# Kernel optimization log

Hardware: AMD Instinct MI355X
Metric: run time of the kernel (lower is better)

The kernel has to match this reference:

```python
import jax, jax.numpy as jnp
import numpy as np

DIM = 192
STATE = 64
B = 8
H = 64
W = 64
EPS_LN = 1e-5
EPS_BN = 1e-5


def _layernorm(x, g, b):
    m = jnp.mean(x, axis=-1, keepdims=True)
    v = jnp.mean((x - m) ** 2, axis=-1, keepdims=True)
    return (x - m) / jnp.sqrt(v + EPS_LN) * g + b


def _linear(x, w, b=None):
    # torch Linear convention: w is [out, in]
    y = jnp.einsum('...i,oi->...o', x, w)
    return y if b is None else y + b


def _parallel_scan(A, Bd, xp):
    # A, Bd, xp: [B, L, S]; h_t = A_t*h_{t-1} + Bd_t*xp_t via log-space cumsum
    A_safe = jnp.clip(A, 0.001, 0.999)
    log_A = jnp.log(A_safe + 1e-10)
    log_cum_A = jnp.cumsum(log_A, axis=1)
    log_cum_A_max = jnp.max(log_cum_A, axis=1, keepdims=True)
    cum_A = jnp.exp(log_cum_A - log_cum_A_max)
    BX = Bd * xp
    # prepend zeros, drop last: normalizer uses cumprod up to t-1
    log_pad = jnp.pad(log_cum_A - log_cum_A_max, ((0, 0), (1, 0), (0, 0)))[:, :-1]
    BX_norm = BX * jnp.exp(-log_pad)
    return jnp.cumsum(BX_norm, axis=1) * cum_A


def _ssm(x, ln_g, ln_b, xp_w, xp_b, dt_w, dt_b, A_log, B_w, C_w, Dp, out_w, out_b):
    xn = _layernorm(x, ln_g, ln_b)
    delta = jax.nn.softplus(_linear(xn, dt_w, dt_b)) * 0.01 + 0.0001  # [B,L,S]
    B_t = _linear(xn, B_w)
    C_t = _linear(xn, C_w)
    A = -jnp.exp(A_log)  # [S]
    x_proj = _linear(xn, xp_w, xp_b)
    deltaA = jnp.clip(delta * A, -10.0, -0.0001)
    A_disc = jnp.exp(deltaA)
    B_disc = delta * B_t
    h = _parallel_scan(A_disc, B_disc, x_proj)
    y = C_t * h
    y = jnp.where(jnp.all(jnp.isfinite(y)), y, jnp.zeros_like(y))
    y = _linear(y, out_w, out_b)
    return y + jnp.clip(Dp, -2.0, 2.0) * x


def reference(x, ln1_g, ln1_b, ln2_g, ln2_b, dw_w, bn_g, bn_b, bn_rm, bn_rv,
              ssm_ln_g, ssm_ln_b, xp_w, xp_b, dt_w, dt_b, A_log, B_w, C_w,
              D_param, out_w, out_b, mlp_w1, mlp_b1, mlp_w2, mlp_b2,
              alpha_local, alpha_ssm, alpha_mlp):
    identity = x
    # depthwise 3x3 conv + BatchNorm2d (eval mode, running stats)
    xc = jax.lax.conv_general_dilated(
        x, dw_w, (1, 1), 'SAME', feature_group_count=DIM,
        dimension_numbers=('NCHW', 'OIHW', 'NCHW'))
    scale = (bn_g / jnp.sqrt(bn_rv + EPS_BN))[None, :, None, None]
    x_local = (xc - bn_rm[None, :, None, None]) * scale + bn_b[None, :, None, None]
    # SSM branch on flattened spatial sequence
    x_seq = x.transpose(0, 2, 3, 1).reshape(B, H * W, DIM)
    x_seq = _layernorm(x_seq, ln1_g, ln1_b)
    x_seq = _ssm(x_seq, ssm_ln_g, ssm_ln_b, xp_w, xp_b, dt_w, dt_b, A_log,
                 B_w, C_w, D_param, out_w, out_b)
    x_ssm = x_seq.reshape(B, H, W, DIM).transpose(0, 3, 1, 2)
    xr = identity + alpha_local * x_local + alpha_ssm * x_ssm
    # residual MLP (dropout = identity at inference)
    x_mlp = xr.transpose(0, 2, 3, 1).reshape(B, H * W, DIM)
    x_mlp = _layernorm(x_mlp, ln2_g, ln2_b)
    x_mlp = _linear(jax.nn.gelu(_linear(x_mlp, mlp_w1, mlp_b1), approximate=False),
                    mlp_w2, mlp_b2)
    return xr + alpha_mlp * x_mlp.reshape(B, H, W, DIM).transpose(0, 3, 1, 2)


def setup_inputs() -> dict:
    key = jax.random.key(0)
    ks = jax.random.split(key, 12)
    def nrm(k, shape, s):
        return jax.random.normal(k, shape, jnp.float32) * s
    f32 = jnp.float32
    return {
        'x': jax.random.normal(ks[0], (B, DIM, H, W), f32),
        'ln1_g': jnp.ones(DIM, f32), 'ln1_b': jnp.zeros(DIM, f32),
        'ln2_g': jnp.ones(DIM, f32), 'ln2_b': jnp.zeros(DIM, f32),
        'dw_w': nrm(ks[1], (DIM, 1, 3, 3), 0.2),
        'bn_g': jnp.ones(DIM, f32), 'bn_b': jnp.zeros(DIM, f32),
        'bn_rm': jnp.zeros(DIM, f32), 'bn_rv': jnp.ones(DIM, f32),
        'ssm_ln_g': jnp.ones(DIM, f32), 'ssm_ln_b': jnp.zeros(DIM, f32),
        'xp_w': nrm(ks[2], (STATE, DIM), 0.05), 'xp_b': jnp.zeros(STATE, f32),
        'dt_w': nrm(ks[3], (STATE, DIM), 0.05), 'dt_b': jnp.zeros(STATE, f32),
        'A_log': jnp.log(jax.random.uniform(ks[4], (STATE,), f32) * 0.8 + 0.2),
        'B_w': nrm(ks[5], (STATE, DIM), 0.05),
        'C_w': nrm(ks[6], (STATE, DIM), 0.05),
        'D_param': jnp.zeros(DIM, f32),
        'out_w': nrm(ks[7], (DIM, STATE), 0.05), 'out_b': jnp.zeros(DIM, f32),
        'mlp_w1': nrm(ks[8], (4 * DIM, DIM), 0.03), 'mlp_b1': jnp.zeros(4 * DIM, f32),
        'mlp_w2': nrm(ks[9], (DIM, 4 * DIM), 0.03), 'mlp_b2': jnp.zeros(DIM, f32),
        'alpha_local': jnp.full((1,), 0.5, f32),
        'alpha_ssm': jnp.full((1,), 0.5, f32),
        'alpha_mlp': jnp.full((1,), 0.5, f32),
    }
```

## Files before the change

### kernel.cpp

```cpp
#include <hip/hip_runtime.h>
#include <hip/hip_bf16.h>
#include <math.h>


#define DEV static __device__ __forceinline__

constexpr int Bn = 8, Dm = 192, Ln = 4096, Sn = 64, Hd = 768;

typedef __attribute__((ext_vector_type(8))) short bf16x8;
typedef __attribute__((ext_vector_type(4))) float f32x4;

DEV float wave_sum(float v) {
#pragma unroll
  for (int off = 1; off < 64; off <<= 1) v += __shfl_xor(v, off);
  return v;
}

DEV short f2b(float x) {
  __hip_bfloat16 h = __float2bfloat16(x);
  return *(short*)&h;
}

DEV float b2f(short x) {
  __hip_bfloat16 h = *(__hip_bfloat16*)&x;
  return __bfloat162float(h);
}

__global__ __launch_bounds__(256) void k_prep(
    const float* __restrict__ x, const float* __restrict__ g1, const float* __restrict__ b1,
    const float* __restrict__ g2, const float* __restrict__ b2,
    short* __restrict__ xnb, short* __restrict__ xln1b,
    const float* __restrict__ dt_w, const float* __restrict__ B_w,
    const float* __restrict__ C_w, const float* __restrict__ xp_w,
    const float* __restrict__ out_w, const float* __restrict__ w1,
    const float* __restrict__ w2, short* __restrict__ wb) {
  __shared__ __align__(16) float tile[Dm * 65];
  int tid = threadIdx.x;
  if (blockIdx.y == 8) {
    for (int i = blockIdx.x * 256 + tid; i < 89088; i += 64 * 256) {
      const float4* src;
      if (i < 3072)       src = (const float4*)dt_w + i;
      else if (i < 6144)  src = (const float4*)B_w + (i - 3072);
      else if (i < 9216)  src = (const float4*)C_w + (i - 6144);
      else if (i < 12288) src = (const float4*)xp_w + (i - 9216);
      else if (i < 15360) src = (const float4*)out_w + (i - 12288);
      else if (i < 52224) src = (const float4*)w1 + (i - 15360);
      else                src = (const float4*)w2 + (i - 52224);
      float4 v = *src;
      int o = i * 4;
      wb[o] = f2b(v.x); wb[o + 1] = f2b(v.y); wb[o + 2] = f2b(v.z); wb[o + 3] = f2b(v.w);
    }
    return;
  }
  int b = blockIdx.y, l0 = blockIdx.x * 64;
  const float* xb = x + (size_t)b * Dm * Ln;
  for (int i = tid; i < Dm * 16; i += 256) {
    int d = i >> 4, l4 = (i & 15) << 2;
    float4 v = *(const float4*)&xb[d * Ln + l0 + l4];
    tile[d * 65 + l4]     = v.x; tile[d * 65 + l4 + 1] = v.y;
    tile[d * 65 + l4 + 2] = v.z; tile[d * 65 + l4 + 3] = v.w;
  }
  __syncthreads();
  int lane = tid & 63, wv = tid >> 6;
  float ga0 = g1[lane], ga1 = g1[lane + 64], ga2 = g1[lane + 128];
  float bb0 = b1[lane], bb1 = b1[lane + 64], bb2 = b1[lane + 128];
  float gc0 = g2[lane], gc1 = g2[lane + 64], gc2 = g2[lane + 128];
  float bc0 = b2[lane], bc1 = b2[lane + 64], bc2 = b2[lane + 128];
  for (int li = wv; li < 64; li += 4) {
    float v0 = tile[lane * 65 + li], v1 = tile[(lane + 64) * 65 + li], v2 = tile[(lane + 128) * 65 + li];
    float s  = wave_sum(v0 + v1 + v2);
    float sq = wave_sum(v0 * v0 + v1 * v1 + v2 * v2);
    float m = s * (1.f / 192.f);
    float inv = rsqrtf(sq * (1.f / 192.f) - m * m + 1e-5f);
    float y0 = (v0 - m) * inv * ga0 + bb0;
    float y1 = (v1 - m) * inv * ga1 + bb1;
    float y2 = (v2 - m) * inv * ga2 + bb2;
    float s2  = wave_sum(y0 + y1 + y2);
    float sq2 = wave_sum(y0 * y0 + y1 * y1 + y2 * y2);
    float m2 = s2 * (1.f / 192.f);
    float inv2 = rsqrtf(sq2 * (1.f / 192.f) - m2 * m2 + 1e-5f);
    size_t base = ((size_t)b * Ln + l0 + li) * Dm;
    xln1b[base + lane]       = f2b(y0);
    xln1b[base + lane + 64]  = f2b(y1);
    xln1b[base + lane + 128] = f2b(y2);
    xnb[base + lane]       = f2b((y0 - m2) * inv2 * gc0 + bc0);
    xnb[base + lane + 64]  = f2b((y1 - m2) * inv2 * gc1 + bc1);
    xnb[base + lane + 128] = f2b((y2 - m2) * inv2 * gc2 + bc2);
  }
}

__global__ __launch_bounds__(256) void k_proj(
    const short* __restrict__ xnb, const short* __restrict__ wcat,
    const float* __restrict__ dt_b, const float* __restrict__ xp_b,
    const float* __restrict__ A_log, float* __restrict__ aA, unsigned* __restrict__ bxc,
    float* __restrict__ sums) {
  __shared__ __align__(16) short As[64 * 72];
  __shared__ __align__(16) short Bs[256 * 72];
  int m0 = blockIdx.x * 64, tid = threadIdx.x;
  int lane = tid & 63, l16 = lane & 15, quad = lane >> 4, w = tid >> 6;
  f32x4 acc[16] = {};
  for (int kt = 0; kt < 3; kt++) {
    int kb = kt * 64;
    for (int i = tid; i < 512; i += 256) {
      int row = i >> 3, c8 = (i & 7) * 8;
      *(float4*)&As[row * 72 + c8] = *(const float4*)&xnb[(size_t)(m0 + row) * 192 + kb + c8];
    }
    for (int i = tid; i < 2048; i += 256) {
      int row = i >> 3, c8 = (i & 7) * 8;
      *(float4*)&Bs[row * 72 + c8] = *(const float4*)&wcat[(size_t)row * 192 + kb + c8];
    }
    __syncthreads();
#pragma unroll
    for (int ks = 0; ks < 2; ks++) {
      int ko = ks * 32 + quad * 8;
      bf16x8 a0 = *(const bf16x8*)&As[(w * 16 + l16) * 72 + ko];
#pragma unroll
      for (int nh = 0; nh < 2; nh++) {
        bf16x8 bfr[8];
#pragma unroll
        for (int j = 0; j < 8; j++) bfr[j] = *(const bf16x8*)&Bs[((nh * 8 + j) * 16 + l16) * 72 + ko];
#pragma unroll
        for (int j = 0; j < 8; j++)
          acc[nh * 8 + j] = __builtin_amdgcn_mfma_f32_16x16x32_bf16(a0, bfr[j], acc[nh * 8 + j], 0, 0, 0);
      }
    }
    __syncthreads();
  }
  float* aAs = (float*)Bs;
  float* bxs = aAs + 64 * 65;
  float Av[4], dtbv[4], xpbv[4];
#pragma unroll
  for (int ni = 0; ni < 4; ni++) {
    int s = ni * 16 + l16;
    Av[ni] = -expf(A_log[s]); dtbv[ni] = dt_b[s]; xpbv[ni] = xp_b[s];
  }
#pragma unroll
  for (int r = 0; r < 4; r++) {
    int lm = w * 16 + quad * 4 + r;
    int m = m0 + lm;
#pragma unroll
    for (int ni = 0; ni < 4; ni++) {
      int s = ni * 16 + l16;
      float z = acc[ni][r] + dtbv[ni];
      float sp = (z > 20.f) ? z : log1pf(expf(z));
      float delta = sp * 0.01f + 0.0001f;
      float bt  = acc[ni + 4][r];
      float ct  = acc[ni + 8][r];
      float xpv = acc[ni + 12][r] + xpbv[ni];
      float dA = fminf(fmaxf(delta * Av[ni], -10.f), -0.0001f);
      float Ae = fminf(fmaxf(expf(dA), 0.001f), 0.999f) + 1e-10f;
      short bxh = f2b(delta * bt * xpv);
      aA[(size_t)m * 64 + s] = Ae;
      unsigned pk = (unsigned)(unsigned short)bxh
                  | ((unsigned)(unsigned short)f2b(ct) << 16);
      bxc[(size_t)m * 64 + s] = pk;
      aAs[lm * 65 + s] = Ae;
      bxs[lm * 65 + s] = b2f(bxh);
    }
  }
  __syncthreads();
  int s = tid & 63, seg = tid >> 6, chunk = seg >> 1, sub = seg & 1;
  bool first = ((m0 & 4095) == 0) && (chunk == 0) && (sub == 0);
  float P = 1.f, H = 0.f;
  int base = chunk * 32 + sub * 16;
#pragma unroll
  for (int j = 0; j < 16; j++) {
    float a  = aAs[(base + j) * 65 + s];
    float bx = bxs[(base + j) * 65 + s];
    if (first && j == 0) { P = a; H = bx; }
    else { P *= a; H = a * (H + bx); }
  }
  float* partP = (float*)As;
  float* partH = partP + 256;
  partP[seg * 64 + s] = P; partH[seg * 64 + s] = H;
  __syncthreads();
  if (tid < 128) {
    int c = tid >> 6;
    float p0 = partP[(c * 2) * 64 + s], p1 = partP[(c * 2 + 1) * 64 + s];
    float h0 = partH[(c * 2) * 64 + s], h1 = partH[(c * 2 + 1) * 64 + s];
    int ci = (m0 >> 12) * 128 + ((m0 & 4095) >> 5) + c;
    sums[(ci * 2 + 0) * 64 + s] = p0 * p1;
    sums[(ci * 2 + 1) * 64 + s] = p1 * h0 + h1;
  }
}

__global__ __launch_bounds__(256) void k_scan2(const float* __restrict__ sums,
                                               float* __restrict__ carries) {
  __shared__ float Pp[4 * 64], Hp[4 * 64];
  int b = blockIdx.x, tid = threadIdx.x, s = tid & 63, q = tid >> 6;
  float P = 1.f, H = 0.f;
#pragma unroll 4
  for (int j = 0; j < 32; j++) {
    int ci = b * 128 + q * 32 + j;
    float a = sums[(ci * 2 + 0) * 64 + s];
    float h = sums[(ci * 2 + 1) * 64 + s];
    P *= a; H = a * H + h;
  }
  Pp[q * 64 + s] = P; Hp[q * 64 + s] = H;
  __syncthreads();
  float cur = 0.f;
  for (int qq = 0; qq < q; qq++) cur = Pp[qq * 64 + s] * cur + Hp[qq * 64 + s];
#pragma unroll 4
  for (int j = 0; j < 32; j++) {
    int ci = b * 128 + q * 32 + j;
    carries[ci * 64 + s] = cur;
    float a = sums[(ci * 2 + 0) * 64 + s];
    float h = sums[(ci * 2 + 1) * 64 + s];
    cur = a * cur + h;
  }
}

__global__ __launch_bounds__(256) void k_out(
    const float* __restrict__ aA, const unsigned* __restrict__ bxc,
    const float* __restrict__ carries,
    const short* __restrict__ owb, const float* __restrict__ out_b,
    const float* __restrict__ Dp, const short* __restrict__ xln1b, float* __restrict__ sout) {
  __shared__ __align__(16) short As[192 * 72];
  __shared__ __align__(16) short Bs[64 * 72];
  int l0g = blockIdx.x * 64, tid = threadIdx.x;
  int lane = tid & 63, l16 = lane & 15, quad = lane >> 4, wv = tid >> 6;
  for (int i = tid; i < 1536; i += 256) {
    int row = i >> 3, c8 = (i & 7) * 8;
    *(float4*)&As[row * 72 + c8] = *(const float4*)&owb[row * 64 + c8];
  }
  int bb = l0g >> 12, c0 = (l0g & 4095) >> 5;
  if (wv < 2) {
    int c = c0 + wv, s = lane;
    float h = carries[(bb * 128 + c) * 64 + s];
    const float* ap = aA + (size_t)(l0g + wv * 32) * 64;
    const unsigned* bp = bxc + (size_t)(l0g + wv * 32) * 64;
    int t = 0;
    if (c == 0) {
      unsigned u = bp[s];
      h = b2f((short)(u & 0xFFFF));
      Bs[(wv * 32) * 72 + s] = f2b(b2f((short)(u >> 16)) * h);
      t = 1;
    }
#pragma unroll 4
    for (; t < 32; t++) {
      unsigned u = bp[t * 64 + s];
      float a = ap[t * 64 + s];
      h = a * (h + b2f((short)(u & 0xFFFF)));
      Bs[(wv * 32 + t) * 72 + s] = f2b(b2f((short)(u >> 16)) * h);
    }
  }
  __syncthreads();
  f32x4 acc[3][4] = {};
#pragma unroll
  for (int ks = 0; ks < 2; ks++) {
    int ko = ks * 32 + quad * 8;
    bf16x8 a[3], b[4];
#pragma unroll
    for (int mi = 0; mi < 3; mi++) a[mi] = *(const bf16x8*)&As[(wv * 48 + mi * 16 + l16) * 72 + ko];
#pragma unroll
    for (int ni = 0; ni < 4; ni++) b[ni] = *(const bf16x8*)&Bs[(ni * 16 + l16) * 72 + ko];
#pragma unroll
    for (int mi = 0; mi < 3; mi++)
#pragma unroll
      for (int ni = 0; ni < 4; ni++)
        acc[mi][ni] = __builtin_amdgcn_mfma_f32_16x16x32_bf16(a[mi], b[ni], acc[mi][ni], 0, 0, 0);
  }
#pragma unroll
  for (int mi = 0; mi < 3; mi++)
#pragma unroll
    for (int r = 0; r < 4; r++) {
      int d = wv * 48 + mi * 16 + quad * 4 + r;
      float ob = out_b[d];
      float dc = fminf(fmaxf(Dp[d], -2.f), 2.f);
#pragma unroll
      for (int ni = 0; ni < 4; ni++) {
        int l = l0g + ni * 16 + l16;
        float v = acc[mi][ni][r] + ob;
        if (dc != 0.f) v += dc * b2f(xln1b[(size_t)l * 192 + d]);
        sout[((size_t)bb * Dm + d) * Ln + (l & 4095)] = v;
      }
    }
}

__global__ __launch_bounds__(256) void k_conv(
    const float* __restrict__ x, const float* __restrict__ dw,
    const float* __restrict__ bn_g, const float* __restrict__ bn_b,
    const float* __restrict__ bn_rm, const float* __restrict__ bn_rv,
    const float* __restrict__ sout, const float* __restrict__ a_loc,
    const float* __restrict__ a_ssm, float* __restrict__ xr) {
  __shared__ __align__(16) float xs[64 * 64];
  int d = blockIdx.x, b = blockIdx.y, tid = threadIdx.x;
  const float* xp = x + ((size_t)b * Dm + d) * Ln;
  for (int i = tid; i < 1024; i += 256) ((float4*)xs)[i] = ((const float4*)xp)[i];
  __syncthreads();
  float w[9];
#pragma unroll
  for (int k = 0; k < 9; k++) w[k] = dw[d * 9 + k];
  float scale = bn_g[d] * rsqrtf(bn_rv[d] + 1e-5f);
  float rm = bn_rm[d], bb = bn_b[d];
  float al = a_loc[0], as_ = a_ssm[0];
  const float* sp = sout + ((size_t)b * Dm + d) * Ln;
  float* xo = xr + ((size_t)b * Dm + d) * Ln;
  for (int i = tid; i < 4096; i += 256) {
    int h = i >> 6, wc = i & 63;
    float acc = 0.f;
#pragma unroll
    for (int kh = 0; kh < 3; kh++) {
      int hh = h + kh - 1;
      if (hh < 0 || hh >= 64) continue;
#pragma unroll
      for (int kw = 0; kw < 3; kw++) {
        int ww2 = wc + kw - 1;
        if (ww2 < 0 || ww2 >= 64) continue;
        acc += xs[hh * 64 + ww2] * w[kh * 3 + kw];
      }
    }
    float xl = (acc - rm) * scale + bb;
    xo[i] = xs[i] + al * xl + as_ * sp[i];
  }
}

__global__ __launch_bounds__(256) void k_ln2(
    const float* __restrict__ xr, const float* __restrict__ g, const float* __restrict__ bb,
    short* __restrict__ xn2) {
  __shared__ __align__(16) float tile[Dm * 65];
  int b = blockIdx.y, l0 = blockIdx.x * 64, tid = threadIdx.x;
  const float* xb = xr + (size_t)b * Dm * Ln;
  for (int i = tid; i < Dm * 16; i += 256) {
    int d = i >> 4, l4 = (i & 15) << 2;
    float4 v = *(const float4*)&xb[d * Ln + l0 + l4];
    tile[d * 65 + l4]     = v.x; tile[d * 65 + l4 + 1] = v.y;
    tile[d * 65 + l4 + 2] = v.z; tile[d * 65 + l4 + 3] = v.w;
  }
  __syncthreads();
  int lane = tid & 63, wv = tid >> 6;
  float g0 = g[lane], g1v = g[lane + 64], g2v = g[lane + 128];
  float b0 = bb[lane], b1v = bb[lane + 64], b2v = bb[lane + 128];
  for (int li = wv; li < 64; li += 4) {
    float v0 = tile[lane * 65 + li], v1 = tile[(lane + 64) * 65 + li], v2 = tile[(lane + 128) * 65 + li];
    float s  = wave_sum(v0 + v1 + v2);
    float sq = wave_sum(v0 * v0 + v1 * v1 + v2 * v2);
    float m = s * (1.f / 192.f);
    float inv = rsqrtf(sq * (1.f / 192.f) - m * m + 1e-5f);
    size_t base = ((size_t)b * Ln + l0 + li) * Dm;
    xn2[base + lane]       = f2b((v0 - m) * inv * g0 + b0);
    xn2[base + lane + 64]  = f2b((v1 - m) * inv * g1v + b1v);
    xn2[base + lane + 128] = f2b((v2 - m) * inv * g2v + b2v);
  }
}

__global__ __launch_bounds__(256) void k_gemm1(
    const short* __restrict__ xn2, const short* __restrict__ w1b,
    const float* __restrict__ b1h, short* __restrict__ hid) {
  __shared__ __align__(16) short smem[2 * 128 * 88];
  short* As = smem;
  short* Bs = smem + 128 * 88;
  int m0 = blockIdx.x * 128, n0 = blockIdx.y * 128, tid = threadIdx.x;
  int lane = tid & 63, l16 = lane & 15, quad = lane >> 4;
  int wm = (tid >> 6) >> 1, wn = (tid >> 6) & 1;
  f32x4 acc[4][4] = {};
  for (int kt = 0; kt < 3; kt++) {
    int kb = kt * 64;
    for (int i = tid; i < 1024; i += 256) {
      int row = i >> 3, c8 = (i & 7) * 8;
      *(float4*)&As[row * 88 + c8] = *(const float4*)&xn2[(size_t)(m0 + row) * 192 + kb + c8];
      *(float4*)&Bs[row * 88 + c8] = *(const float4*)&w1b[(size_t)(n0 + row) * 192 + kb + c8];
    }
    __syncthreads();
#pragma unroll
    for (int ks = 0; ks < 2; ks++) {
      int ko = ks * 32 + quad * 8;
      bf16x8 a[4], b[4];
#pragma unroll
      for (int mi = 0; mi < 4; mi++) a[mi] = *(const bf16x8*)&As[(wm * 64 + mi * 16 + l16) * 88 + ko];
#pragma unroll
      for (int ni = 0; ni < 4; ni++) b[ni] = *(const bf16x8*)&Bs[(wn * 64 + ni * 16 + l16) * 88 + ko];
#pragma unroll
      for (int mi = 0; mi < 4; mi++)
#pragma unroll
        for (int ni = 0; ni < 4; ni++)
          acc[mi][ni] = __builtin_amdgcn_mfma_f32_16x16x32_bf16(a[mi], b[ni], acc[mi][ni], 0, 0, 0);
    }
    __syncthreads();
  }
  short* Cs = smem;
  float bias4[4];
#pragma unroll
  for (int ni = 0; ni < 4; ni++) bias4[ni] = b1h[n0 + wn * 64 + ni * 16 + l16];
#pragma unroll
  for (int mi = 0; mi < 4; mi++)
#pragma unroll
    for (int ni = 0; ni < 4; ni++) {
      int n = wn * 64 + ni * 16 + l16;
#pragma unroll
      for (int r = 0; r < 4; r++) {
        int m = wm * 64 + mi * 16 + quad * 4 + r;
        float v = acc[mi][ni][r] + bias4[ni];
        float g = 0.5f * v * (1.f + erff(v * 0.70710678118f));
        Cs[m * 136 + n] = f2b(g);
      }
    }
  __syncthreads();
  for (int i = tid; i < 2048; i += 256) {
    int m = i >> 4, ch = i & 15;
    *(float4*)&hid[(size_t)(m0 + m) * 768 + n0 + ch * 8] = *(const float4*)&Cs[m * 136 + ch * 8];
  }
}

__global__ __launch_bounds__(256) void k_gemm2(
    const short* __restrict__ hid, const short* __restrict__ w2b,
    const float* __restrict__ b2o, const float* __restrict__ xr,
    const float* __restrict__ am, float* __restrict__ out) {
  __shared__ __align__(16) short Wt[96 * 88];
  __shared__ __align__(16) short Ht[64 * 88];
  int l0g = blockIdx.x * 64, d0 = blockIdx.y * 96, tid = threadIdx.x;
  int lane = tid & 63, l16 = lane & 15, quad = lane >> 4;
  int wm = (tid >> 6) >> 1, wn = (tid >> 6) & 1;
  f32x4 acc[3][2] = {};
  for (int kt = 0; kt < 12; kt++) {
    int kb = kt * 64;
    for (int i = tid; i < 768; i += 256) {
      int row = i >> 3, c8 = (i & 7) * 8;
      *(float4*)&Wt[row * 88 + c8] = *(const float4*)&w2b[(size_t)(d0 + row) * 768 + kb + c8];
    }
    for (int i = tid; i < 512; i += 256) {
      int row = i >> 3, c8 = (i & 7) * 8;
      *(float4*)&Ht[row * 88 + c8] = *(const float4*)&hid[(size_t)(l0g + row) * 768 + kb + c8];
    }
    __syncthreads();
#pragma unroll
    for (int ks = 0; ks < 2; ks++) {
      int ko = ks * 32 + quad * 8;
      bf16x8 a[3], b[2];
#pragma unroll
      for (int mi = 0; mi < 3; mi++) a[mi] = *(const bf16x8*)&Wt[(wm * 48 + mi * 16 + l16) * 88 + ko];
#pragma unroll
      for (int ni = 0; ni < 2; ni++) b[ni] = *(const bf16x8*)&Ht[(wn * 32 + ni * 16 + l16) * 88 + ko];
#pragma unroll
      for (int mi = 0; mi < 3; mi++)
#pragma unroll
        for (int ni = 0; ni < 2; ni++)
          acc[mi][ni] = __builtin_amdgcn_mfma_f32_16x16x32_bf16(a[mi], b[ni], acc[mi][ni], 0, 0, 0);
    }
    __syncthreads();
  }
  float alpha = am[0];
#pragma unroll
  for (int mi = 0; mi < 3; mi++)
#pragma unroll
    for (int r = 0; r < 4; r++) {
      int d = d0 + wm * 48 + mi * 16 + quad * 4 + r;
      float bias = b2o[d];
#pragma unroll
      for (int ni = 0; ni < 2; ni++) {
        int lg = l0g + wn * 32 + ni * 16 + l16;
        size_t idx = ((size_t)(lg >> 12) * Dm + d) * Ln + (lg & 4095);
        out[idx] = xr[idx] + alpha * (acc[mi][ni][r] + bias);
      }
    }
}

extern "C" void kernel_launch(void* const* d_in, const int* in_sizes, int n_in,
                              void* d_out, int out_size, void* d_ws, size_t ws_size,
                              hipStream_t stream) {
  (void)in_sizes; (void)n_in; (void)out_size; (void)ws_size;
  const float* x     = (const float*)d_in[0];
  const float* ln1_g = (const float*)d_in[1];
  const float* ln1_b = (const float*)d_in[2];
  const float* ln2_g = (const float*)d_in[3];
  const float* ln2_b = (const float*)d_in[4];
  const float* dw_w  = (const float*)d_in[5];
  const float* bn_g  = (const float*)d_in[6];
  const float* bn_b  = (const float*)d_in[7];
  const float* bn_rm = (const float*)d_in[8];
  const float* bn_rv = (const float*)d_in[9];
  const float* ssm_g = (const float*)d_in[10];
  const float* ssm_b = (const float*)d_in[11];
  const float* xp_w  = (const float*)d_in[12];
  const float* xp_b  = (const float*)d_in[13];
  const float* dt_w  = (const float*)d_in[14];
  const float* dt_b  = (const float*)d_in[15];
  const float* A_log = (const float*)d_in[16];
  const float* B_w   = (const float*)d_in[17];
  const float* C_w   = (const float*)d_in[18];
  const float* Dp    = (const float*)d_in[19];
  const float* out_w = (const float*)d_in[20];
  const float* out_b = (const float*)d_in[21];
  const float* w1    = (const float*)d_in[22];
  const float* b1    = (const float*)d_in[23];
  const float* w2    = (const float*)d_in[24];
  const float* b2    = (const float*)d_in[25];
  const float* a_loc = (const float*)d_in[26];
  const float* a_ssm = (const float*)d_in[27];
  const float* a_mlp = (const float*)d_in[28];

  float* ws = (float*)d_ws;
  short*    xnb   = (short*)ws;
  short*    xln1b = (short*)(ws + 3145728);
  float*    aA    = ws + 6291456;
  unsigned* bxc   = (unsigned*)(ws + 8388608);
  float*    sout  = ws + 11534336;
  float*    xr    = ws + 17825792;
  short*    wb    = (short*)(ws + 24117248);
  float*    sums  = ws + 24829952;
  float*    carr  = ws + 24961024;
  short*    xn2   = (short*)(ws + 25026560);
  short*    hid   = (short*)(ws + 28172288);
  short*    wcatb = wb;
  short*    owb   = wb + 49152;
  short*    w1b   = wb + 61440;
  short*    w2b   = wb + 208896;
  float*    out   = (float*)d_out;

  k_prep <<<dim3(64, 9),  256, 0, stream>>>(x, ln1_g, ln1_b, ssm_g, ssm_b, xnb, xln1b,
                                            dt_w, B_w, C_w, xp_w, out_w, w1, w2, wb);
  k_proj <<<dim3(512),    256, 0, stream>>>(xnb, wcatb, dt_b, xp_b, A_log, aA, bxc, sums);
  k_scan2<<<dim3(8),      256, 0, stream>>>(sums, carr);
  k_out  <<<dim3(512),    256, 0, stream>>>(aA, bxc, carr, owb, out_b, Dp, xln1b, sout);
  k_conv <<<dim3(192, 8), 256, 0, stream>>>(x, dw_w, bn_g, bn_b, bn_rm, bn_rv, sout, a_loc, a_ssm, xr);
  k_ln2  <<<dim3(64, 8),  256, 0, stream>>>(xr, ln2_g, ln2_b, xn2);
  k_gemm1<<<dim3(256, 6), 256, 0, stream>>>(xn2, w1b, b1, hid);
  k_gemm2<<<dim3(512, 2), 256, 0, stream>>>(hid, w2b, b2, xr, a_mlp, out);
}
```

Before: 271.7 us.

## Fuse SSM residual add and LayerNorm2 into k_out, run conv first

```diff
diff --git a/kernel.cpp b/kernel.cpp
--- a/kernel.cpp
+++ b/kernel.cpp
@@ -210,13 +210,54 @@
   }
 }
 
+__global__ __launch_bounds__(256) void k_conv(
+    const float* __restrict__ x, const float* __restrict__ dw,
+    const float* __restrict__ bn_g, const float* __restrict__ bn_b,
+    const float* __restrict__ bn_rm, const float* __restrict__ bn_rv,
+    const float* __restrict__ a_loc, float* __restrict__ xr) {
+  __shared__ __align__(16) float xs[64 * 64];
+  int d = blockIdx.x, b = blockIdx.y, tid = threadIdx.x;
+  const float* xp = x + ((size_t)b * Dm + d) * Ln;
+  for (int i = tid; i < 1024; i += 256) ((float4*)xs)[i] = ((const float4*)xp)[i];
+  __syncthreads();
+  float w[9];
+#pragma unroll
+  for (int k = 0; k < 9; k++) w[k] = dw[d * 9 + k];
+  float scale = bn_g[d] * rsqrtf(bn_rv[d] + 1e-5f);
+  float rm = bn_rm[d], bb = bn_b[d];
+  float al = a_loc[0];
+  float* xo = xr + ((size_t)b * Dm + d) * Ln;
+  for (int i = tid; i < 4096; i += 256) {
+    int h = i >> 6, wc = i & 63;
+    float acc = 0.f;
+#pragma unroll
+    for (int kh = 0; kh < 3; kh++) {
+      int hh = h + kh - 1;
+      if (hh < 0 || hh >= 64) continue;
+#pragma unroll
+      for (int kw = 0; kw < 3; kw++) {
+        int ww2 = wc + kw - 1;
+        if (ww2 < 0 || ww2 >= 64) continue;
+        acc += xs[hh * 64 + ww2] * w[kh * 3 + kw];
+      }
+    }
+    float xl = (acc - rm) * scale + bb;
+    xo[i] = xs[i] + al * xl;
+  }
+}
+
 __global__ __launch_bounds__(256) void k_out(
     const float* __restrict__ aA, const unsigned* __restrict__ bxc,
     const float* __restrict__ carries,
     const short* __restrict__ owb, const float* __restrict__ out_b,
-    const float* __restrict__ Dp, const short* __restrict__ xln1b, float* __restrict__ sout) {
-  __shared__ __align__(16) short As[192 * 72];
-  __shared__ __align__(16) short Bs[64 * 72];
+    const float* __restrict__ Dp, const short* __restrict__ xln1b,
+    const float* __restrict__ a_ssm, const float* __restrict__ g2,
+    const float* __restrict__ bb2,
+    float* __restrict__ xr, short* __restrict__ xn2) {
+  __shared__ __align__(16) float smemf[64 * 193];
+  short* As = (short*)smemf;
+  short* Bs = (short*)smemf + 192 * 72;
+  float* tile = smemf;
   int l0g = blockIdx.x * 64, tid = threadIdx.x;
   int lane = tid & 63, l16 = lane & 15, quad = lane >> 4, wv = tid >> 6;
   for (int i = tid; i < 1536; i += 256) {
@@ -260,6 +301,8 @@
       for (int ni = 0; ni < 4; ni++)
         acc[mi][ni] = __builtin_amdgcn_mfma_f32_16x16x32_bf16(a[mi], b[ni], acc[mi][ni], 0, 0, 0);
   }
+  __syncthreads();
+  float as_ = a_ssm[0];
 #pragma unroll
   for (int mi = 0; mi < 3; mi++)
 #pragma unroll
@@ -272,72 +315,22 @@
         int l = l0g + ni * 16 + l16;
         float v = acc[mi][ni][r] + ob;
         if (dc != 0.f) v += dc * b2f(xln1b[(size_t)l * 192 + d]);
-        sout[((size_t)bb * Dm + d) * Ln + (l & 4095)] = v;
+        size_t idx = ((size_t)bb * Dm + d) * Ln + (l & 4095);
+        float nx = xr[idx] + as_ * v;
+        xr[idx] = nx;
+        tile[(l & 63) * 193 + d] = nx;
       }
     }
-}
-
-__global__ __launch_bounds__(256) void k_conv(
-    const float* __restrict__ x, const float* __restrict__ dw,
-    const float* __restrict__ bn_g, const float* __restrict__ bn_b,
-    const float* __restrict__ bn_rm, const float* __restrict__ bn_rv,
-    const float* __restrict__ sout, const float* __restrict__ a_loc,
-    const float* __restrict__ a_ssm, float* __restrict__ xr) {
-  __shared__ __align__(16) float xs[64 * 64];
-  int d = blockIdx.x, b = blockIdx.y, tid = threadIdx.x;
-  const float* xp = x + ((size_t)b * Dm + d) * Ln;
-  for (int i = tid; i < 1024; i += 256) ((float4*)xs)[i] = ((const float4*)xp)[i];
-  __syncthreads();
-  float w[9];
-#pragma unroll
-  for (int k = 0; k < 9; k++) w[k] = dw[d * 9 + k];
-  float scale = bn_g[d] * rsqrtf(bn_rv[d] + 1e-5f);
-  float rm = bn_rm[d], bb = bn_b[d];
-  float al = a_loc[0], as_ = a_ssm[0];
-  const float* sp = sout + ((size_t)b * Dm + d) * Ln;
-  float* xo = xr + ((size_t)b * Dm + d) * Ln;
-  for (int i = tid; i < 4096; i += 256) {
-    int h = i >> 6, wc = i & 63;
-    float acc = 0.f;
-#pragma unroll
-    for (int kh = 0; kh < 3; kh++) {
-      int hh = h + kh - 1;
-      if (hh < 0 || hh >= 64) continue;
-#pragma unroll
-      for (int kw = 0; kw < 3; kw++) {
-        int ww2 = wc + kw - 1;
-        if (ww2 < 0 || ww2 >= 64) continue;
-        acc += xs[hh * 64 + ww2] * w[kh * 3 + kw];
-      }
-    }
-    float xl = (acc - rm) * scale + bb;
-    xo[i] = xs[i] + al * xl + as_ * sp[i];
-  }
-}
-
-__global__ __launch_bounds__(256) void k_ln2(
-    const float* __restrict__ xr, const float* __restrict__ g, const float* __restrict__ bb,
-    short* __restrict__ xn2) {
-  __shared__ __align__(16) float tile[Dm * 65];
-  int b = blockIdx.y, l0 = blockIdx.x * 64, tid = threadIdx.x;
-  const float* xb = xr + (size_t)b * Dm * Ln;
-  for (int i = tid; i < Dm * 16; i += 256) {
-    int d = i >> 4, l4 = (i & 15) << 2;
-    float4 v = *(const float4*)&xb[d * Ln + l0 + l4];
-    tile[d * 65 + l4]     = v.x; tile[d * 65 + l4 + 1] = v.y;
-    tile[d * 65 + l4 + 2] = v.z; tile[d * 65 + l4 + 3] = v.w;
-  }
-  __syncthreads();
-  int lane = tid & 63, wv = tid >> 6;
-  float g0 = g[lane], g1v = g[lane + 64], g2v = g[lane + 128];
-  float b0 = bb[lane], b1v = bb[lane + 64], b2v = bb[lane + 128];
+  __syncthreads();
+  float g0 = g2[lane], g1v = g2[lane + 64], g2v = g2[lane + 128];
+  float b0 = bb2[lane], b1v = bb2[lane + 64], b2v = bb2[lane + 128];
   for (int li = wv; li < 64; li += 4) {
-    float v0 = tile[lane * 65 + li], v1 = tile[(lane + 64) * 65 + li], v2 = tile[(lane + 128) * 65 + li];
+    float v0 = tile[li * 193 + lane], v1 = tile[li * 193 + lane + 64], v2 = tile[li * 193 + lane + 128];
     float s  = wave_sum(v0 + v1 + v2);
     float sq = wave_sum(v0 * v0 + v1 * v1 + v2 * v2);
     float m = s * (1.f / 192.f);
     float inv = rsqrtf(sq * (1.f / 192.f) - m * m + 1e-5f);
-    size_t base = ((size_t)b * Ln + l0 + li) * Dm;
+    size_t base = (size_t)(l0g + li) * Dm;
     xn2[base + lane]       = f2b((v0 - m) * inv * g0 + b0);
     xn2[base + lane + 64]  = f2b((v1 - m) * inv * g1v + b1v);
     xn2[base + lane + 128] = f2b((v2 - m) * inv * g2v + b2v);
@@ -494,7 +487,6 @@
   short*    xln1b = (short*)(ws + 3145728);
   float*    aA    = ws + 6291456;
   unsigned* bxc   = (unsigned*)(ws + 8388608);
-  float*    sout  = ws + 11534336;
   float*    xr    = ws + 17825792;
   short*    wb    = (short*)(ws + 24117248);
   float*    sums  = ws + 24829952;
@@ -509,11 +501,11 @@
 
   k_prep <<<dim3(64, 9),  256, 0, stream>>>(x, ln1_g, ln1_b, ssm_g, ssm_b, xnb, xln1b,
                                             dt_w, B_w, C_w, xp_w, out_w, w1, w2, wb);
+  k_conv <<<dim3(192, 8), 256, 0, stream>>>(x, dw_w, bn_g, bn_b, bn_rm, bn_rv, a_loc, xr);
   k_proj <<<dim3(512),    256, 0, stream>>>(xnb, wcatb, dt_b, xp_b, A_log, aA, bxc, sums);
   k_scan2<<<dim3(8),      256, 0, stream>>>(sums, carr);
-  k_out  <<<dim3(512),    256, 0, stream>>>(aA, bxc, carr, owb, out_b, Dp, xln1b, sout);
-  k_conv <<<dim3(192, 8), 256, 0, stream>>>(x, dw_w, bn_g, bn_b, bn_rm, bn_rv, sout, a_loc, a_ssm, xr);
-  k_ln2  <<<dim3(64, 8),  256, 0, stream>>>(xr, ln2_g, ln2_b, xn2);
+  k_out  <<<dim3(512),    256, 0, stream>>>(aA, bxc, carr, owb, out_b, Dp, xln1b,
+                                            a_ssm, ln2_g, ln2_b, xr, xn2);
   k_gemm1<<<dim3(256, 6), 256, 0, stream>>>(xn2, w1b, b1, hid);
   k_gemm2<<<dim3(512, 2), 256, 0, stream>>>(hid, w2b, b2, xr, a_mlp, out);
 }
```

Result: no change. 276.6 us (+1.8%).
